# Optimization experiments

Measured on AMD Instinct MI355X. Metric: run time of the kernel, lower is better.

The kernel has to match this reference:

```python
import jax, jax.numpy as jnp
import numpy as np

N_NODES = 100000
N_EDGES = 3200000
IN_DIM = 128
HID = 16
MEM = 16
N_LAYERS = 2
OUT = 2
SLOPE = 0.01  # torch leaky_relu default negative_slope


def setup_inputs() -> dict:
    key = jax.random.key(0)
    ks = jax.random.split(key, 20)
    s = 0.05
    inp = {
        "x": jax.random.normal(ks[0], (N_NODES, IN_DIM), dtype=jnp.float32),
        "edge_index": jax.random.randint(ks[1], (2, N_EDGES), 0, N_NODES, dtype=jnp.int64),
        # preprocess MLP: Linear(input_dim,256) -> Linear(256,hidden)
        "pre1_W": jax.random.normal(ks[2], (256, IN_DIM), dtype=jnp.float32) * s,
        "pre1_b": jax.random.normal(ks[3], (256,), dtype=jnp.float32) * s,
        "pre2_W": jax.random.normal(ks[4], (HID, 256), dtype=jnp.float32) * s,
        "pre2_b": jax.random.normal(ks[5], (HID,), dtype=jnp.float32) * s,
        # per-layer hypernetwork GRU biases (input & initial hidden are zeros, so
        # only biases affect the GRU step) and weight_transform Linear(mem, hid*hid)
        "gru_bih": jax.random.normal(ks[6], (N_LAYERS, 3 * MEM), dtype=jnp.float32) * s,
        "gru_bhh": jax.random.normal(ks[7], (N_LAYERS, 3 * MEM), dtype=jnp.float32) * s,
        "wt_W": jax.random.normal(ks[8], (N_LAYERS, HID * HID, MEM), dtype=jnp.float32) * s,
        "wt_b": jax.random.normal(ks[9], (N_LAYERS, HID * HID), dtype=jnp.float32) * s,
        # GCNConv bias (kept as its own parameter in PyG; lin has bias=False)
        "gcn_b": jax.random.normal(ks[10], (N_LAYERS, HID), dtype=jnp.float32) * s,
        # postprocess heads
        "post1_W": jax.random.normal(ks[11], (OUT, HID), dtype=jnp.float32) * s,
        "post1_b": jax.random.normal(ks[12], (OUT,), dtype=jnp.float32) * s,
        "posta_W": jax.random.normal(ks[13], (1, HID), dtype=jnp.float32) * s,
        "posta_b": jax.random.normal(ks[14], (1,), dtype=jnp.float32) * s,
    }
    return inp


def _hyper_gcn_weight(bih, bhh, wt_W, wt_b):
    # GRU single step with zero input and zero initial hidden state:
    # only the biases contribute.  h' = (1-z)*n + z*h_prev, h_prev = 0.
    r = jax.nn.sigmoid(bih[:MEM] + bhh[:MEM])
    z = jax.nn.sigmoid(bih[MEM:2 * MEM] + bhh[MEM:2 * MEM])
    n = jnp.tanh(bih[2 * MEM:] + r * bhh[2 * MEM:])
    mem = (1.0 - z) * n  # [MEM]
    # weight_transform Linear -> view as lin.weight [out, in]; detached in torch
    W = (wt_W @ mem + wt_b).reshape(HID, HID)
    return jax.lax.stop_gradient(W)


def reference(x, edge_index, pre1_W, pre1_b, pre2_W, pre2_b, gru_bih, gru_bhh,
              wt_W, wt_b, gcn_b, post1_W, post1_b, posta_W, posta_b):
    N = x.shape[0]
    # preprocess (dropout p=0.0 -> identity)
    h = jax.nn.leaky_relu(x @ pre1_W.T + pre1_b, negative_slope=SLOPE)
    h = jax.nn.leaky_relu(h @ pre2_W.T + pre2_b, negative_slope=SLOPE)

    # GCN normalization with self-loops (PyG gcn_norm)
    src, dst = edge_index[0], edge_index[1]
    loops = jnp.arange(N, dtype=src.dtype)
    s = jnp.concatenate([src, loops])
    d = jnp.concatenate([dst, loops])
    deg = jax.ops.segment_sum(jnp.ones_like(d, dtype=h.dtype), d, num_segments=N)
    dinv = jnp.where(deg > 0, jax.lax.rsqrt(deg), 0.0)
    norm = dinv[s] * dinv[d]  # [E+N]

    for l in range(N_LAYERS):
        W = _hyper_gcn_weight(gru_bih[l], gru_bhh[l], wt_W[l], wt_b[l])
        xw = h @ W.T                                   # [N, HID]
        msg = xw[s] * norm[:, None]                    # gather + scale
        h = jax.ops.segment_sum(msg, d, num_segments=N) + gcn_b[l]
        h = jax.nn.leaky_relu(h, negative_slope=SLOPE)

    out = jnp.sum(h @ post1_W.T + post1_b, axis=-1)          # [N]
    anomaly = (h @ posta_W.T + posta_b)[:, 0]                # [N]
    return out, anomaly, h
```

## Files before the change

kernel.cpp:

```cpp
#include <hip/hip_runtime.h>
#include <hip/hip_bf16.h>
#include <math.h>

#define IN_DIM 128
#define PRE_HID 256
#define HID 16

__device__ __forceinline__ float lrelu(float v) { return v > 0.f ? v : 0.01f * v; }
__device__ __forceinline__ float fin(float v) { return (v == v && fabsf(v) < 1e30f) ? v : 0.f; }

__device__ __forceinline__ float ldp(const void* p, size_t i, int f32) {
    if (f32) return ((const float*)p)[i];
    unsigned u = ((const unsigned short*)p)[i];
    return __uint_as_float(u << 16);
}
__device__ __forceinline__ unsigned short f2bf(float f) {
    union { __hip_bfloat16 b; unsigned short u; } cv;
    cv.b = __float2bfloat16(f);
    return cv.u;
}
__device__ __forceinline__ void unpack8(uint4 u, float* o) {
    o[0] = __uint_as_float(u.x << 16); o[1] = __uint_as_float(u.x & 0xFFFF0000u);
    o[2] = __uint_as_float(u.y << 16); o[3] = __uint_as_float(u.y & 0xFFFF0000u);
    o[4] = __uint_as_float(u.z << 16); o[5] = __uint_as_float(u.z & 0xFFFF0000u);
    o[6] = __uint_as_float(u.w << 16); o[7] = __uint_as_float(u.w & 0xFFFF0000u);
}
__device__ __forceinline__ unsigned pk2(float a, float b) {
    return (unsigned)f2bf(a) | ((unsigned)f2bf(b) << 16);
}
__device__ __forceinline__ uint4 pack8(const float* v) {
    uint4 u;
    u.x = pk2(v[0], v[1]); u.y = pk2(v[2], v[3]);
    u.z = pk2(v[4], v[5]); u.w = pk2(v[6], v[7]);
    return u;
}

#define OFF_W1F   0
#define OFF_B1F   32768
#define OFF_W2T   33024
#define OFF_B2F   37120
#define OFF_HW    37136
#define OFF_GCNB  37648
#define OFF_POST  37680
#define OFF_FLAGS 37720
#define OFF_BSUM  37760
#define OFF_BPRE  37888
#define OFF_A0    38016

__global__ void k_detect(const unsigned short* __restrict__ xu,
                         const int* __restrict__ ei32, int* __restrict__ flags) {
    if (threadIdx.x == 0 && blockIdx.x == 0) {
        int band = 0;
        for (int k = 0; k < 128; ++k) {
            unsigned e = (xu[2 * k] >> 7) & 0xFF;
            if (e >= 100 && e <= 140) band++;
        }
        flags[1] = (band < 96) ? 1 : 0;
        int any = 0;
        for (int k = 0; k < 64; ++k) any |= ei32[2 * k + 1];
        flags[0] = (any == 0) ? 1 : 0;
    }
}

__global__ void k_sentinel(unsigned* __restrict__ out, int words, unsigned val) {
    int i = blockIdx.x * 256 + threadIdx.x;
    if (i < words) out[i] = val;
}

__global__ void k_prep_small(const void* __restrict__ bih, const void* __restrict__ bhh,
                             const void* __restrict__ wtW, const void* __restrict__ wtb,
                             const void* __restrict__ p1W, const void* __restrict__ p1b,
                             const void* __restrict__ paW, const void* __restrict__ pab,
                             const int* __restrict__ flags,
                             float* __restrict__ hw, float* __restrict__ post) {
    int f32 = flags[1];
    __shared__ float mem[2][16];
    int t = threadIdx.x;
    if (t < 32) {
        int l = t >> 4, j = t & 15;
        float bi0 = ldp(bih, l * 48 + j, f32),      bh0 = ldp(bhh, l * 48 + j, f32);
        float bi1 = ldp(bih, l * 48 + 16 + j, f32), bh1 = ldp(bhh, l * 48 + 16 + j, f32);
        float bi2 = ldp(bih, l * 48 + 32 + j, f32), bh2 = ldp(bhh, l * 48 + 32 + j, f32);
        float r = 1.f / (1.f + expf(-(bi0 + bh0)));
        float z = 1.f / (1.f + expf(-(bi1 + bh1)));
        float nn = tanhf(bi2 + r * bh2);
        mem[l][j] = (1.f - z) * nn;
    }
    __syncthreads();
    for (int l = 0; l < 2; ++l) {
        float acc = ldp(wtb, l * 256 + t, f32);
        #pragma unroll
        for (int m = 0; m < 16; ++m)
            acc += ldp(wtW, l * 4096 + t * 16 + m, f32) * mem[l][m];
        hw[l * 256 + t] = acc;
    }
    if (t < 16) {
        post[t]      = ldp(p1W, t, f32) + ldp(p1W, 16 + t, f32);
        post[17 + t] = ldp(paW, t, f32);
    }
    if (t == 0) {
        post[16] = ldp(p1b, 0, f32) + ldp(p1b, 1, f32);
        post[33] = ldp(pab, 0, f32);
    }
}

__global__ void k_convert(const void* __restrict__ p1W, const void* __restrict__ p1b,
                          const void* __restrict__ p2W, const void* __restrict__ p2b,
                          const void* __restrict__ gcnb, const int* __restrict__ flags,
                          float* __restrict__ w1f, float* __restrict__ b1f,
                          float* __restrict__ w2t, float* __restrict__ b2f,
                          float* __restrict__ gcnbf) {
    int f32 = flags[1];
    int i = blockIdx.x * 256 + threadIdx.x;
    if (i < 32768) w1f[i] = ldp(p1W, i, f32);
    if (i < 256)   b1f[i] = ldp(p1b, i, f32);
    if (i < 4096)  { int r = i >> 4, j = i & 15; w2t[i] = ldp(p2W, j * 256 + r, f32); }
    if (i < 16)    b2f[i] = ldp(p2b, i, f32);
    if (i < 32)    gcnbf[i] = ldp(gcnb, i, f32);
}

__global__ void k_deg(const int* __restrict__ ei, const int* __restrict__ flags,
                      unsigned* __restrict__ deg, int E, int N) {
    int e = blockIdx.x * 256 + threadIdx.x;
    if (e >= E) return;
    int d = flags[0] ? ei[2 * ((size_t)E + e)] : ei[(size_t)E + e];
    if ((unsigned)d < (unsigned)N) atomicAdd(&deg[d], 1u);
}

__global__ void k_dinv(float* __restrict__ degdinv, int N) {
    int n = blockIdx.x * 256 + threadIdx.x;
    if (n >= N) return;
    unsigned dg = ((unsigned*)degdinv)[n];
    degdinv[n] = 1.f / sqrtf((float)dg + 1.f);
}

__global__ void k_dinv2(const unsigned* __restrict__ deg, float* __restrict__ dinv, int N) {
    int n = blockIdx.x * 256 + threadIdx.x;
    if (n >= N) return;
    dinv[n] = 1.f / sqrtf((float)deg[n] + 1.f);
}

__global__ __launch_bounds__(1024) void k_scan_block(const unsigned* __restrict__ deg,
                                                     unsigned* __restrict__ bsum, int N) {
    __shared__ unsigned s[1024];
    int t = threadIdx.x;
    int i = blockIdx.x * 1024 + t;
    s[t] = (i < N) ? deg[i] : 0u;
    __syncthreads();
    for (int off = 512; off > 0; off >>= 1) {
        if (t < off) s[t] += s[t + off];
        __syncthreads();
    }
    if (t == 0) bsum[blockIdx.x] = s[0];
}

__global__ __launch_bounds__(128) void k_scan_top(unsigned* __restrict__ bsum,
                                                  unsigned* __restrict__ bpre, int NB) {
    __shared__ unsigned s[128];
    int t = threadIdx.x;
    unsigned v = (t < NB) ? bsum[t] : 0u;
    s[t] = v;
    __syncthreads();
    for (int off = 1; off < 128; off <<= 1) {
        unsigned a = (t >= off) ? s[t - off] : 0u;
        __syncthreads();
        s[t] += a;
        __syncthreads();
    }
    if (t < NB) bpre[t] = s[t] - v;
}

__global__ __launch_bounds__(1024) void k_scan_final(const unsigned* __restrict__ deg,
                                                     const unsigned* __restrict__ bpre,
                                                     unsigned* __restrict__ rowptr, int N) {
    __shared__ unsigned s[1024];
    int t = threadIdx.x;
    int i = blockIdx.x * 1024 + t;
    unsigned v = (i < N) ? deg[i] : 0u;
    s[t] = v;
    __syncthreads();
    for (int off = 1; off < 1024; off <<= 1) {
        unsigned a = (t >= off) ? s[t - off] : 0u;
        __syncthreads();
        s[t] += a;
        __syncthreads();
    }
    if (i < N) rowptr[i] = bpre[blockIdx.x] + s[t] - v;
}

__global__ void k_fill(const int* __restrict__ ei, const int* __restrict__ flags,
                       unsigned* __restrict__ rowptr, unsigned* __restrict__ csr,
                       int E, int N) {
    int e = blockIdx.x * 256 + threadIdx.x;
    if (e >= E) return;
    int s, d;
    if (flags[0]) { s = ei[2 * (size_t)e]; d = ei[2 * ((size_t)E + e)]; }
    else          { s = ei[e];             d = ei[(size_t)E + e]; }
    if ((unsigned)d >= (unsigned)N) return;
    if ((unsigned)s >= (unsigned)N) s = d;
    unsigned pos = atomicAdd(&rowptr[d], 1u);
    csr[pos] = (unsigned)s;
}

__global__ __launch_bounds__(256) void k_pre(const void* __restrict__ x,
                                             const float* __restrict__ w1f,
                                             const float* __restrict__ b1f,
                                             const float* __restrict__ w2t,
                                             const float* __restrict__ b2f,
                                             const int* __restrict__ flags,
                                             float* __restrict__ h, int N) {
    __shared__ unsigned short xs[64 * 128];
    __shared__ float pacc[192 * 16];
    const int t = threadIdx.x;
    const int base = blockIdx.x * 64;
    const int f32 = flags[1];
    #pragma unroll
    for (int i = 0; i < 4; ++i) {
        int id = i * 256 + t;
        int row = id >> 4, c = id & 15;
        uint4 v = make_uint4(0u, 0u, 0u, 0u);
        if (base + row < N) {
            if (f32) {
                const float* xp = (const float*)x + ((size_t)(base + row) << 7) + c * 8;
                float4 a = *reinterpret_cast<const float4*>(xp);
                float4 b = *reinterpret_cast<const float4*>(xp + 4);
                v.x = pk2(a.x, a.y); v.y = pk2(a.z, a.w);
                v.z = pk2(b.x, b.y); v.w = pk2(b.z, b.w);
            } else {
                v = *reinterpret_cast<const uint4*>((const unsigned short*)x +
                                                    ((size_t)(base + row) << 7) + c * 8);
            }
        }
        int cs = c ^ (row & 15);
        *reinterpret_cast<uint4*>(xs + row * 128 + cs * 8) = v;
    }
    __syncthreads();

    const int node = t & 63;
    const int half = t >> 6;
    const int rowbase = half * 64;
    const int nm = node & 15;

    float acc2[HID];
    #pragma unroll
    for (int j = 0; j < HID; ++j) acc2[j] = (half == 0) ? b2f[j] : 0.f;

    for (int rt = 0; rt < 8; ++rt) {
        const int r0 = rowbase + rt * 8;
        float s[8];
        #pragma unroll
        for (int r = 0; r < 8; ++r) s[r] = b1f[r0 + r];
        #pragma unroll 4
        for (int kc = 0; kc < 16; ++kc) {
            int cs = kc ^ nm;
            uint4 u = *reinterpret_cast<const uint4*>(xs + node * 128 + cs * 8);
            float xr[8];
            unpack8(u, xr);
            const float* wbase = w1f + (size_t)r0 * IN_DIM + kc * 8;
            #pragma unroll
            for (int r = 0; r < 8; ++r) {
                const float* wr = wbase + (size_t)r * IN_DIM;
                float acc = s[r];
                #pragma unroll
                for (int k = 0; k < 8; ++k) acc += wr[k] * xr[k];
                s[r] = acc;
            }
        }
        const float* w2base = w2t + (size_t)r0 * HID;
        #pragma unroll
        for (int r = 0; r < 8; ++r) {
            float v = lrelu(s[r]);
            const float* w2r = w2base + (size_t)r * HID;
            #pragma unroll
            for (int j = 0; j < HID; ++j) acc2[j] += w2r[j] * v;
        }
    }

    if (half != 0) {
        float* pp = pacc + ((half - 1) * 64 + node) * 16;
        #pragma unroll
        for (int j = 0; j < HID; ++j) pp[j] = acc2[j];
    }
    __syncthreads();
    if (half == 0 && base + node < N) {
        const float* p0 = pacc + node * 16;
        const float* p1 = pacc + (64 + node) * 16;
        const float* p2 = pacc + (128 + node) * 16;
        float4* hp = reinterpret_cast<float4*>(h + (size_t)(base + node) * HID);
        #pragma unroll
        for (int q = 0; q < 4; ++q) {
            float4 v;
            v.x = lrelu(acc2[q*4+0] + p0[q*4+0] + p1[q*4+0] + p2[q*4+0]);
            v.y = lrelu(acc2[q*4+1] + p0[q*4+1] + p1[q*4+1] + p2[q*4+1]);
            v.z = lrelu(acc2[q*4+2] + p0[q*4+2] + p1[q*4+2] + p2[q*4+2]);
            v.w = lrelu(acc2[q*4+3] + p0[q*4+3] + p1[q*4+3] + p2[q*4+3]);
            hp[q] = v;
        }
    }
}

__global__ void k_xw_y(const float* __restrict__ h, const float* __restrict__ W,
                       const float* __restrict__ dinv, float* __restrict__ y, int N) {
    int n = blockIdx.x * 256 + threadIdx.x;
    if (n >= N) return;
    float hv[HID];
    const float4* hp = reinterpret_cast<const float4*>(h + (size_t)n * HID);
    #pragma unroll
    for (int q = 0; q < 4; ++q) {
        float4 v = hp[q];
        hv[q*4+0] = v.x; hv[q*4+1] = v.y; hv[q*4+2] = v.z; hv[q*4+3] = v.w;
    }
    float dn = dinv[n];
    float4* yp = reinterpret_cast<float4*>(y + (size_t)n * HID);
    #pragma unroll
    for (int q = 0; q < 4; ++q) {
        float o[4];
        #pragma unroll
        for (int ii = 0; ii < 4; ++ii) {
            int i = q * 4 + ii;
            float s = 0.f;
            #pragma unroll
            for (int j = 0; j < HID; ++j) s += W[i * HID + j] * hv[j];
            o[ii] = s * dn;
        }
        float4 v; v.x = o[0]; v.y = o[1]; v.z = o[2]; v.w = o[3];
        yp[q] = v;
    }
}

__global__ __launch_bounds__(256) void k_gather(const unsigned* __restrict__ rowptr,
                                                const unsigned* __restrict__ deg,
                                                const unsigned* __restrict__ csr,
                                                const float* __restrict__ y,
                                                const float* __restrict__ dinv,
                                                const float* __restrict__ gcnbf,
                                                float* __restrict__ h, int N) {
    int tid = blockIdx.x * 256 + threadIdx.x;
    if (tid >= N * 4) return;
    int n = tid >> 2, q = tid & 3;
    unsigned end = rowptr[n];
    unsigned start = end - deg[n];
    float4 acc = *reinterpret_cast<const float4*>(y + (size_t)n * HID + q * 4);
    unsigned k = start;
    if (k < end) {
        unsigned src = csr[k];
        for (++k; k < end; ++k) {
            unsigned nxt = csr[k];
            float4 v = *reinterpret_cast<const float4*>(y + (size_t)src * HID + q * 4);
            acc.x += v.x; acc.y += v.y; acc.z += v.z; acc.w += v.w;
            src = nxt;
        }
        float4 v = *reinterpret_cast<const float4*>(y + (size_t)src * HID + q * 4);
        acc.x += v.x; acc.y += v.y; acc.z += v.z; acc.w += v.w;
    }
    float dn = dinv[n];
    float4 o;
    o.x = lrelu(fin(dn * acc.x) + gcnbf[q*4+0]);
    o.y = lrelu(fin(dn * acc.y) + gcnbf[q*4+1]);
    o.z = lrelu(fin(dn * acc.z) + gcnbf[q*4+2]);
    o.w = lrelu(fin(dn * acc.w) + gcnbf[q*4+3]);
    *reinterpret_cast<float4*>(h + (size_t)n * HID + q * 4) = o;
}

__global__ __launch_bounds__(256) void k_gather_final(const unsigned* __restrict__ rowptr,
                                                      const unsigned* __restrict__ deg,
                                                      const unsigned* __restrict__ csr,
                                                      const float* __restrict__ y,
                                                      const float* __restrict__ dinv,
                                                      const float* __restrict__ gcnbf,
                                                      const float* __restrict__ post,
                                                      const int* __restrict__ flags,
                                                      void* __restrict__ out, int N) {
    int tid = blockIdx.x * 256 + threadIdx.x;
    if (tid >= N * 4) return;
    int n = tid >> 2, q = tid & 3;
    unsigned end = rowptr[n];
    unsigned start = end - deg[n];
    float4 acc = *reinterpret_cast<const float4*>(y + (size_t)n * HID + q * 4);
    unsigned k = start;
    if (k < end) {
        unsigned src = csr[k];
        for (++k; k < end; ++k) {
            unsigned nxt = csr[k];
            float4 v = *reinterpret_cast<const float4*>(y + (size_t)src * HID + q * 4);
            acc.x += v.x; acc.y += v.y; acc.z += v.z; acc.w += v.w;
            src = nxt;
        }
        float4 v = *reinterpret_cast<const float4*>(y + (size_t)src * HID + q * 4);
        acc.x += v.x; acc.y += v.y; acc.z += v.z; acc.w += v.w;
    }
    float dn = dinv[n];
    float v0 = lrelu(fin(dn * acc.x) + gcnbf[q*4+0]);
    float v1 = lrelu(fin(dn * acc.y) + gcnbf[q*4+1]);
    float v2 = lrelu(fin(dn * acc.z) + gcnbf[q*4+2]);
    float v3 = lrelu(fin(dn * acc.w) + gcnbf[q*4+3]);
    float s1 = v0 * post[q*4+0] + v1 * post[q*4+1] + v2 * post[q*4+2] + v3 * post[q*4+3];
    float s2 = v0 * post[17+q*4+0] + v1 * post[17+q*4+1] + v2 * post[17+q*4+2] + v3 * post[17+q*4+3];
    #pragma unroll
    for (int m = 1; m < 4; m <<= 1) {
        s1 += __shfl_xor(s1, m, 64);
        s2 += __shfl_xor(s2, m, 64);
    }
    if (flags[1]) {
        float* ob = (float*)out;
        if (q == 0) ob[n] = s1 + post[16];
        if (q == 1) ob[N + n] = s2 + post[33];
        float4 o; o.x = v0; o.y = v1; o.z = v2; o.w = v3;
        *reinterpret_cast<float4*>(ob + 2 * (size_t)N + (size_t)n * HID + q * 4) = o;
    } else {
        unsigned short* ob = (unsigned short*)out;
        if (q == 0) ob[n] = f2bf(s1 + post[16]);
        if (q == 1) ob[N + n] = f2bf(s2 + post[33]);
        uint2 u; u.x = pk2(v0, v1); u.y = pk2(v2, v3);
        *reinterpret_cast<uint2*>(ob + 2 * (size_t)N + (size_t)n * HID + q * 4) = u;
    }
}

__global__ void k_xw(const float* __restrict__ h, const float* __restrict__ W,
                     const float* __restrict__ dinv, const int* __restrict__ flags,
                     void* __restrict__ xw, float* __restrict__ hacc, int N) {
    int n = blockIdx.x * 256 + threadIdx.x;
    if (n >= N) return;
    float hv[HID];
    const float4* hp = reinterpret_cast<const float4*>(h + (size_t)n * HID);
    #pragma unroll
    for (int q = 0; q < 4; ++q) {
        float4 v = hp[q];
        hv[q*4+0] = v.x; hv[q*4+1] = v.y; hv[q*4+2] = v.z; hv[q*4+3] = v.w;
    }
    float dn = dinv[n];
    float sl = dn * dn;
    float o[HID];
    #pragma unroll
    for (int i = 0; i < HID; ++i) {
        float s = 0.f;
        #pragma unroll
        for (int j = 0; j < HID; ++j) s += W[i * HID + j] * hv[j];
        o[i] = s;
    }
    if (flags[1]) {
        float4* xp = reinterpret_cast<float4*>((float*)xw + (size_t)n * HID);
        #pragma unroll
        for (int q = 0; q < 4; ++q) {
            float4 v; v.x = o[q*4+0]; v.y = o[q*4+1]; v.z = o[q*4+2]; v.w = o[q*4+3];
            xp[q] = v;
        }
    } else {
        uint4* xp = reinterpret_cast<uint4*>((unsigned short*)xw + (size_t)n * HID);
        xp[0] = pack8(o);
        xp[1] = pack8(o + 8);
    }
    float4* ap = reinterpret_cast<float4*>(hacc + (size_t)n * HID);
    #pragma unroll
    for (int q = 0; q < 4; ++q) {
        float4 va;
        va.x = o[q*4+0]*sl; va.y = o[q*4+1]*sl; va.z = o[q*4+2]*sl; va.w = o[q*4+3]*sl;
        ap[q] = va;
    }
}

__global__ __launch_bounds__(256) void k_scatter(const int* __restrict__ ei,
                                                 const int* __restrict__ flags,
                                                 const float* __restrict__ dinv,
                                                 const void* __restrict__ xw,
                                                 float* __restrict__ hacc, int E, int N) {
    int e = blockIdx.x * 256 + threadIdx.x;
    if (e >= E) return;
    int s, d;
    if (flags[0]) { s = ei[2 * (size_t)e]; d = ei[2 * ((size_t)E + e)]; }
    else          { s = ei[e];             d = ei[(size_t)E + e]; }
    if ((unsigned)s >= (unsigned)N || (unsigned)d >= (unsigned)N) return;
    float nrm = dinv[s] * dinv[d];
    float v[HID];
    if (flags[1]) {
        const float4* xr = reinterpret_cast<const float4*>((const float*)xw + (size_t)s * HID);
        #pragma unroll
        for (int q = 0; q < 4; ++q) {
            float4 a = xr[q];
            v[q*4+0] = a.x; v[q*4+1] = a.y; v[q*4+2] = a.z; v[q*4+3] = a.w;
        }
    } else {
        const uint4* xr = reinterpret_cast<const uint4*>((const unsigned short*)xw + (size_t)s * HID);
        unpack8(xr[0], v);
        unpack8(xr[1], v + 8);
    }
    float* out = hacc + (size_t)d * HID;
    #pragma unroll
    for (int j = 0; j < HID; ++j) unsafeAtomicAdd(out + j, v[j] * nrm);
}

__global__ void k_finish(const float* __restrict__ hacc, const float* __restrict__ gcnbf,
                         float* __restrict__ h, int N) {
    int n = blockIdx.x * 256 + threadIdx.x;
    if (n >= N) return;
    const float4* ap = reinterpret_cast<const float4*>(hacc + (size_t)n * HID);
    float4* hp = reinterpret_cast<float4*>(h + (size_t)n * HID);
    #pragma unroll
    for (int q = 0; q < 4; ++q) {
        float4 a = ap[q];
        float4 o;
        o.x = lrelu(fin(a.x) + gcnbf[q*4+0]);
        o.y = lrelu(fin(a.y) + gcnbf[q*4+1]);
        o.z = lrelu(fin(a.z) + gcnbf[q*4+2]);
        o.w = lrelu(fin(a.w) + gcnbf[q*4+3]);
        hp[q] = o;
    }
}

__global__ void k_final(const float* __restrict__ hacc, const float* __restrict__ gcnbf,
                        const float* __restrict__ post, const int* __restrict__ flags,
                        void* __restrict__ out, int N) {
    int n = blockIdx.x * 256 + threadIdx.x;
    if (n >= N) return;
    float v[HID];
    const float4* ap = reinterpret_cast<const float4*>(hacc + (size_t)n * HID);
    #pragma unroll
    for (int q = 0; q < 4; ++q) {
        float4 a = ap[q];
        v[q*4+0] = lrelu(fin(a.x) + gcnbf[q*4+0]);
        v[q*4+1] = lrelu(fin(a.y) + gcnbf[q*4+1]);
        v[q*4+2] = lrelu(fin(a.z) + gcnbf[q*4+2]);
        v[q*4+3] = lrelu(fin(a.w) + gcnbf[q*4+3]);
    }
    float o = post[16], an = post[33];
    #pragma unroll
    for (int j = 0; j < HID; ++j) {
        o += v[j] * post[j];
        an += v[j] * post[17 + j];
    }
    if (flags[1]) {
        float* ob = (float*)out;
        ob[n] = o;
        ob[N + n] = an;
        float* hr = ob + 2 * (size_t)N + (size_t)n * HID;
        #pragma unroll
        for (int j = 0; j < HID; ++j) hr[j] = v[j];
    } else {
        unsigned short* ob = (unsigned short*)out;
        ob[n] = f2bf(o);
        ob[N + n] = f2bf(an);
        uint4* hr = reinterpret_cast<uint4*>(ob + 2 * (size_t)N + (size_t)n * HID);
        hr[0] = pack8(v);
        hr[1] = pack8(v + 8);
    }
}

extern "C" void kernel_launch(void* const* d_in, const int* in_sizes, int n_in,
                              void* d_out, int out_size, void* d_ws, size_t ws_size,
                              hipStream_t stream) {
    const void* x    = d_in[0];
    const int*  ei   = (const int*)d_in[1];
    const void* p1W  = d_in[2];
    const void* p1b  = d_in[3];
    const void* p2W  = d_in[4];
    const void* p2b  = d_in[5];
    const void* bih  = d_in[6];
    const void* bhh  = d_in[7];
    const void* wtW  = d_in[8];
    const void* wtb  = d_in[9];
    const void* gcnb = d_in[10];
    const void* po1W = d_in[11];
    const void* po1b = d_in[12];
    const void* poaW = d_in[13];
    const void* poab = d_in[14];

    const int N = in_sizes[0] / IN_DIM;
    const int E = in_sizes[1] / 2;

    float* ws = (float*)d_ws;
    float* w1f   = ws + OFF_W1F;
    float* b1f   = ws + OFF_B1F;
    float* w2t   = ws + OFF_W2T;
    float* b2f   = ws + OFF_B2F;
    float* hw    = ws + OFF_HW;
    float* gcnbf = ws + OFF_GCNB;
    float* post  = ws + OFF_POST;
    int*   flags = (int*)(ws + OFF_FLAGS);
    unsigned* bsum = (unsigned*)(ws + OFF_BSUM);
    unsigned* bpre = (unsigned*)(ws + OFF_BPRE);

    const int nb_nodes = (N + 255) / 256;
    const int nb_edges = (E + 255) / 256;
    const int nb_n4    = (N * 4 + 255) / 256;
    const int nb_pre   = (N + 63) / 64;
    const int NB       = (N + 1023) / 1024;

    size_t req_csr = ((size_t)OFF_A0 + 35 * (size_t)N + (size_t)E + 64) * 4;
    size_t req_fb  = ((size_t)OFF_A0 + 33 * (size_t)N + 64) * 4;

    if (ws_size >= req_csr && NB <= 128) {
        unsigned* deg    = (unsigned*)(ws + OFF_A0);
        unsigned* rowptr = deg + N;
        float*    dinv   = (float*)(rowptr + N);
        unsigned* csr    = (unsigned*)(dinv + N);
        float*    y      = (float*)(csr + E);
        float*    h      = y + (size_t)N * HID;

        hipMemsetAsync(deg, 0, (size_t)N * 4, stream);
        k_detect<<<1, 64, 0, stream>>>((const unsigned short*)x, ei, flags);
        k_prep_small<<<1, 256, 0, stream>>>(bih, bhh, wtW, wtb, po1W, po1b, poaW, poab,
                                            flags, hw, post);
        k_convert<<<128, 256, 0, stream>>>(p1W, p1b, p2W, p2b, gcnb, flags,
                                           w1f, b1f, w2t, b2f, gcnbf);
        k_deg<<<nb_edges, 256, 0, stream>>>(ei, flags, deg, E, N);
        k_dinv2<<<nb_nodes, 256, 0, stream>>>(deg, dinv, N);
        k_scan_block<<<NB, 1024, 0, stream>>>(deg, bsum, N);
        k_scan_top<<<1, 128, 0, stream>>>(bsum, bpre, NB);
        k_scan_final<<<NB, 1024, 0, stream>>>(deg, bpre, rowptr, N);
        k_fill<<<nb_edges, 256, 0, stream>>>(ei, flags, rowptr, csr, E, N);
        k_pre<<<nb_pre, 256, 0, stream>>>(x, w1f, b1f, w2t, b2f, flags, h, N);

        k_xw_y<<<nb_nodes, 256, 0, stream>>>(h, hw + 0, dinv, y, N);
        k_gather<<<nb_n4, 256, 0, stream>>>(rowptr, deg, csr, y, dinv, gcnbf + 0, h, N);
        k_xw_y<<<nb_nodes, 256, 0, stream>>>(h, hw + 256, dinv, y, N);
        k_gather_final<<<nb_n4, 256, 0, stream>>>(rowptr, deg, csr, y, dinv, gcnbf + 16,
                                                  post, flags, d_out, N);
    } else if (ws_size >= req_fb) {
        float* degdinv = ws + OFF_A0;
        float* hacc    = degdinv + N;
        float* h       = hacc + (size_t)N * HID;
        void*  xw      = d_out;

        hipMemsetAsync(degdinv, 0, (size_t)N * 4, stream);
        k_detect<<<1, 64, 0, stream>>>((const unsigned short*)x, ei, flags);
        k_prep_small<<<1, 256, 0, stream>>>(bih, bhh, wtW, wtb, po1W, po1b, poaW, poab,
                                            flags, hw, post);
        k_convert<<<128, 256, 0, stream>>>(p1W, p1b, p2W, p2b, gcnb, flags,
                                           w1f, b1f, w2t, b2f, gcnbf);
        k_deg<<<nb_edges, 256, 0, stream>>>(ei, flags, (unsigned*)degdinv, E, N);
        k_dinv<<<nb_nodes, 256, 0, stream>>>(degdinv, N);
        k_pre<<<nb_pre, 256, 0, stream>>>(x, w1f, b1f, w2t, b2f, flags, h, N);
        for (int l = 0; l < 2; ++l) {
            k_xw<<<nb_nodes, 256, 0, stream>>>(h, hw + l * 256, degdinv, flags, xw, hacc, N);
            k_scatter<<<nb_edges, 256, 0, stream>>>(ei, flags, degdinv, xw, hacc, E, N);
            if (l == 0) k_finish<<<nb_nodes, 256, 0, stream>>>(hacc, gcnbf + 0, h, N);
            else        k_final<<<nb_nodes, 256, 0, stream>>>(hacc, gcnbf + 16, post, flags, d_out, N);
        }
    } else {
        float f = 256.0f + (float)(ws_size >> 20);
        unsigned uv; __builtin_memcpy(&uv, &f, 4);
        int words = out_size / 2;
        k_sentinel<<<(words + 255) / 256, 256, 0, stream>>>((unsigned*)d_out, words, uv);
    }
}
```

Before: 1.130 ms.

## Fuse per-layer XW transform into preprocess and gather kernels

Folds the first layer's h·W and dinv scaling into the preprocess MLP kernel and the second layer's into the layer-1 gather epilogue, removing both k_xw_y launches and the h round trips through memory. The preprocess kernel also remaps threads so the four partial sums for a node sit in adjacent lanes and are combined with wavefront shuffles instead of shared memory and a barrier. The gather uses shuffles within groups of four lanes to assemble the full 16-wide row before the matvec. The costs are more register pressure and a change in the memory access pattern for x in shared memory (adjacent lanes now read different swizzled rows).

```diff
diff --git a/kernel.cpp b/kernel.cpp
--- a/kernel.cpp
+++ b/kernel.cpp
@@ -207,10 +207,11 @@
                                              const float* __restrict__ b1f,
                                              const float* __restrict__ w2t,
                                              const float* __restrict__ b2f,
+                                             const float* __restrict__ W0,
+                                             const float* __restrict__ dinv,
                                              const int* __restrict__ flags,
-                                             float* __restrict__ h, int N) {
+                                             float* __restrict__ y, int N) {
     __shared__ unsigned short xs[64 * 128];
-    __shared__ float pacc[192 * 16];
     const int t = threadIdx.x;
     const int base = blockIdx.x * 64;
     const int f32 = flags[1];
@@ -236,14 +237,14 @@
     }
     __syncthreads();
 
-    const int node = t & 63;
-    const int half = t >> 6;
+    const int node = t >> 2;
+    const int half = t & 3;
     const int rowbase = half * 64;
     const int nm = node & 15;
 
     float acc2[HID];
     #pragma unroll
-    for (int j = 0; j < HID; ++j) acc2[j] = (half == 0) ? b2f[j] : 0.f;
+    for (int j = 0; j < HID; ++j) acc2[j] = 0.f;
 
     for (int rt = 0; rt < 8; ++rt) {
         const int r0 = rowbase + rt * 8;
@@ -275,91 +276,87 @@
             for (int j = 0; j < HID; ++j) acc2[j] += w2r[j] * v;
         }
     }
-
-    if (half != 0) {
-        float* pp = pacc + ((half - 1) * 64 + node) * 16;
-        #pragma unroll
-        for (int j = 0; j < HID; ++j) pp[j] = acc2[j];
-    }
-    __syncthreads();
+    #pragma unroll
+    for (int j = 0; j < HID; ++j) {
+        acc2[j] += __shfl_xor(acc2[j], 1, 64);
+        acc2[j] += __shfl_xor(acc2[j], 2, 64);
+    }
     if (half == 0 && base + node < N) {
-        const float* p0 = pacc + node * 16;
-        const float* p1 = pacc + (64 + node) * 16;
-        const float* p2 = pacc + (128 + node) * 16;
-        float4* hp = reinterpret_cast<float4*>(h + (size_t)(base + node) * HID);
+        int n = base + node;
+        float hv[HID];
+        #pragma unroll
+        for (int j = 0; j < HID; ++j) hv[j] = lrelu(acc2[j] + b2f[j]);
+        float dn = dinv[n];
+        float4* yp = reinterpret_cast<float4*>(y + (size_t)n * HID);
         #pragma unroll
         for (int q = 0; q < 4; ++q) {
-            float4 v;
-            v.x = lrelu(acc2[q*4+0] + p0[q*4+0] + p1[q*4+0] + p2[q*4+0]);
-            v.y = lrelu(acc2[q*4+1] + p0[q*4+1] + p1[q*4+1] + p2[q*4+1]);
-            v.z = lrelu(acc2[q*4+2] + p0[q*4+2] + p1[q*4+2] + p2[q*4+2]);
-            v.w = lrelu(acc2[q*4+3] + p0[q*4+3] + p1[q*4+3] + p2[q*4+3]);
-            hp[q] = v;
-        }
-    }
-}
-
-__global__ void k_xw_y(const float* __restrict__ h, const float* __restrict__ W,
-                       const float* __restrict__ dinv, float* __restrict__ y, int N) {
-    int n = blockIdx.x * 256 + threadIdx.x;
-    if (n >= N) return;
-    float hv[HID];
-    const float4* hp = reinterpret_cast<const float4*>(h + (size_t)n * HID);
-    #pragma unroll
-    for (int q = 0; q < 4; ++q) {
-        float4 v = hp[q];
-        hv[q*4+0] = v.x; hv[q*4+1] = v.y; hv[q*4+2] = v.z; hv[q*4+3] = v.w;
-    }
-    float dn = dinv[n];
-    float4* yp = reinterpret_cast<float4*>(y + (size_t)n * HID);
-    #pragma unroll
-    for (int q = 0; q < 4; ++q) {
-        float o[4];
-        #pragma unroll
-        for (int ii = 0; ii < 4; ++ii) {
-            int i = q * 4 + ii;
-            float s = 0.f;
+            float o[4];
             #pragma unroll
-            for (int j = 0; j < HID; ++j) s += W[i * HID + j] * hv[j];
-            o[ii] = s * dn;
-        }
-        float4 v; v.x = o[0]; v.y = o[1]; v.z = o[2]; v.w = o[3];
-        yp[q] = v;
+            for (int ii = 0; ii < 4; ++ii) {
+                int i = q * 4 + ii;
+                float s = 0.f;
+                #pragma unroll
+                for (int j = 0; j < HID; ++j) s += W0[i * HID + j] * hv[j];
+                o[ii] = s * dn;
+            }
+            float4 v; v.x = o[0]; v.y = o[1]; v.z = o[2]; v.w = o[3];
+            yp[q] = v;
+        }
     }
 }
 
 __global__ __launch_bounds__(256) void k_gather(const unsigned* __restrict__ rowptr,
                                                 const unsigned* __restrict__ deg,
                                                 const unsigned* __restrict__ csr,
-                                                const float* __restrict__ y,
+                                                const float* __restrict__ ya,
                                                 const float* __restrict__ dinv,
                                                 const float* __restrict__ gcnbf,
-                                                float* __restrict__ h, int N) {
+                                                const float* __restrict__ W,
+                                                float* __restrict__ yb, int N) {
     int tid = blockIdx.x * 256 + threadIdx.x;
     if (tid >= N * 4) return;
     int n = tid >> 2, q = tid & 3;
     unsigned end = rowptr[n];
     unsigned start = end - deg[n];
-    float4 acc = *reinterpret_cast<const float4*>(y + (size_t)n * HID + q * 4);
+    float4 acc = *reinterpret_cast<const float4*>(ya + (size_t)n * HID + q * 4);
     unsigned k = start;
     if (k < end) {
         unsigned src = csr[k];
         for (++k; k < end; ++k) {
             unsigned nxt = csr[k];
-            float4 v = *reinterpret_cast<const float4*>(y + (size_t)src * HID + q * 4);
+            float4 v = *reinterpret_cast<const float4*>(ya + (size_t)src * HID + q * 4);
             acc.x += v.x; acc.y += v.y; acc.z += v.z; acc.w += v.w;
             src = nxt;
         }
-        float4 v = *reinterpret_cast<const float4*>(y + (size_t)src * HID + q * 4);
+        float4 v = *reinterpret_cast<const float4*>(ya + (size_t)src * HID + q * 4);
         acc.x += v.x; acc.y += v.y; acc.z += v.z; acc.w += v.w;
     }
     float dn = dinv[n];
-    float4 o;
-    o.x = lrelu(fin(dn * acc.x) + gcnbf[q*4+0]);
-    o.y = lrelu(fin(dn * acc.y) + gcnbf[q*4+1]);
-    o.z = lrelu(fin(dn * acc.z) + gcnbf[q*4+2]);
-    o.w = lrelu(fin(dn * acc.w) + gcnbf[q*4+3]);
-    *reinterpret_cast<float4*>(h + (size_t)n * HID + q * 4) = o;
+    float v0 = lrelu(fin(dn * acc.x) + gcnbf[q*4+0]);
+    float v1 = lrelu(fin(dn * acc.y) + gcnbf[q*4+1]);
+    float v2 = lrelu(fin(dn * acc.z) + gcnbf[q*4+2]);
+    float v3 = lrelu(fin(dn * acc.w) + gcnbf[q*4+3]);
+    int lb = (threadIdx.x & 63) & ~3;
+    float hrow[HID];
+    #pragma unroll
+    for (int k2 = 0; k2 < 4; ++k2) {
+        int sl = lb + k2;
+        hrow[k2*4+0] = __shfl(v0, sl, 64);
+        hrow[k2*4+1] = __shfl(v1, sl, 64);
+        hrow[k2*4+2] = __shfl(v2, sl, 64);
+        hrow[k2*4+3] = __shfl(v3, sl, 64);
+    }
+    float o[4];
+    #pragma unroll
+    for (int ii = 0; ii < 4; ++ii) {
+        int i = q * 4 + ii;
+        float s = 0.f;
+        #pragma unroll
+        for (int j = 0; j < HID; ++j) s += W[i * HID + j] * hrow[j];
+        o[ii] = s * dn;
+    }
+    float4 ov; ov.x = o[0]; ov.y = o[1]; ov.z = o[2]; ov.w = o[3];
+    *reinterpret_cast<float4*>(yb + (size_t)n * HID + q * 4) = ov;
 }
 
 __global__ __launch_bounds__(256) void k_gather_final(const unsigned* __restrict__ rowptr,
@@ -416,6 +413,99 @@
     }
 }
 
+__global__ __launch_bounds__(256) void k_pre_fb(const void* __restrict__ x,
+                                                const float* __restrict__ w1f,
+                                                const float* __restrict__ b1f,
+                                                const float* __restrict__ w2t,
+                                                const float* __restrict__ b2f,
+                                                const int* __restrict__ flags,
+                                                float* __restrict__ h, int N) {
+    __shared__ unsigned short xs[64 * 128];
+    __shared__ float pacc[192 * 16];
+    const int t = threadIdx.x;
+    const int base = blockIdx.x * 64;
+    const int f32 = flags[1];
+    #pragma unroll
+    for (int i = 0; i < 4; ++i) {
+        int id = i * 256 + t;
+        int row = id >> 4, c = id & 15;
+        uint4 v = make_uint4(0u, 0u, 0u, 0u);
+        if (base + row < N) {
+            if (f32) {
+                const float* xp = (const float*)x + ((size_t)(base + row) << 7) + c * 8;
+                float4 a = *reinterpret_cast<const float4*>(xp);
+                float4 b = *reinterpret_cast<const float4*>(xp + 4);
+                v.x = pk2(a.x, a.y); v.y = pk2(a.z, a.w);
+                v.z = pk2(b.x, b.y); v.w = pk2(b.z, b.w);
+            } else {
+                v = *reinterpret_cast<const uint4*>((const unsigned short*)x +
+                                                    ((size_t)(base + row) << 7) + c * 8);
+            }
+        }
+        int cs = c ^ (row & 15);
+        *reinterpret_cast<uint4*>(xs + row * 128 + cs * 8) = v;
+    }
+    __syncthreads();
+    const int node = t & 63;
+    const int half = t >> 6;
+    const int rowbase = half * 64;
+    const int nm = node & 15;
+    float acc2[HID];
+    #pragma unroll
+    for (int j = 0; j < HID; ++j) acc2[j] = (half == 0) ? b2f[j] : 0.f;
+    for (int rt = 0; rt < 8; ++rt) {
+        const int r0 = rowbase + rt * 8;
+        float s[8];
+        #pragma unroll
+        for (int r = 0; r < 8; ++r) s[r] = b1f[r0 + r];
+        #pragma unroll 4
+        for (int kc = 0; kc < 16; ++kc) {
+            int cs = kc ^ nm;
+            uint4 u = *reinterpret_cast<const uint4*>(xs + node * 128 + cs * 8);
+            float xr[8];
+            unpack8(u, xr);
+            const float* wbase = w1f + (size_t)r0 * IN_DIM + kc * 8;
+            #pragma unroll
+            for (int r = 0; r < 8; ++r) {
+                const float* wr = wbase + (size_t)r * IN_DIM;
+                float acc = s[r];
+                #pragma unroll
+                for (int k = 0; k < 8; ++k) acc += wr[k] * xr[k];
+                s[r] = acc;
+            }
+        }
+        const float* w2base = w2t + (size_t)r0 * HID;
+        #pragma unroll
+        for (int r = 0; r < 8; ++r) {
+            float v = lrelu(s[r]);
+            const float* w2r = w2base + (size_t)r * HID;
+            #pragma unroll
+            for (int j = 0; j < HID; ++j) acc2[j] += w2r[j] * v;
+        }
+    }
+    if (half != 0) {
+        float* pp = pacc + ((half - 1) * 64 + node) * 16;
+        #pragma unroll
+        for (int j = 0; j < HID; ++j) pp[j] = acc2[j];
+    }
+    __syncthreads();
+    if (half == 0 && base + node < N) {
+        const float* p0 = pacc + node * 16;
+        const float* p1 = pacc + (64 + node) * 16;
+        const float* p2 = pacc + (128 + node) * 16;
+        float4* hp = reinterpret_cast<float4*>(h + (size_t)(base + node) * HID);
+        #pragma unroll
+        for (int q = 0; q < 4; ++q) {
+            float4 v;
+            v.x = lrelu(acc2[q*4+0] + p0[q*4+0] + p1[q*4+0] + p2[q*4+0]);
+            v.y = lrelu(acc2[q*4+1] + p0[q*4+1] + p1[q*4+1] + p2[q*4+1]);
+            v.z = lrelu(acc2[q*4+2] + p0[q*4+2] + p1[q*4+2] + p2[q*4+2]);
+            v.w = lrelu(acc2[q*4+3] + p0[q*4+3] + p1[q*4+3] + p2[q*4+3]);
+            hp[q] = v;
+        }
+    }
+}
+
 __global__ void k_xw(const float* __restrict__ h, const float* __restrict__ W,
                      const float* __restrict__ dinv, const int* __restrict__ flags,
                      void* __restrict__ xw, float* __restrict__ hacc, int N) {
@@ -593,8 +683,8 @@
         unsigned* rowptr = deg + N;
         float*    dinv   = (float*)(rowptr + N);
         unsigned* csr    = (unsigned*)(dinv + N);
-        float*    y      = (float*)(csr + E);
-        float*    h      = y + (size_t)N * HID;
+        float*    ya     = (float*)(csr + E);
+        float*    yb     = ya + (size_t)N * HID;
 
         hipMemsetAsync(deg, 0, (size_t)N * 4, stream);
         k_detect<<<1, 64, 0, stream>>>((const unsigned short*)x, ei, flags);
@@ -608,12 +698,11 @@
         k_scan_top<<<1, 128, 0, stream>>>(bsum, bpre, NB);
         k_scan_final<<<NB, 1024, 0, stream>>>(deg, bpre, rowptr, N);
         k_fill<<<nb_edges, 256, 0, stream>>>(ei, flags, rowptr, csr, E, N);
-        k_pre<<<nb_pre, 256, 0, stream>>>(x, w1f, b1f, w2t, b2f, flags, h, N);
-
-        k_xw_y<<<nb_nodes, 256, 0, stream>>>(h, hw + 0, dinv, y, N);
-        k_gather<<<nb_n4, 256, 0, stream>>>(rowptr, deg, csr, y, dinv, gcnbf + 0, h, N);
-        k_xw_y<<<nb_nodes, 256, 0, stream>>>(h, hw + 256, dinv, y, N);
-        k_gather_final<<<nb_n4, 256, 0, stream>>>(rowptr, deg, csr, y, dinv, gcnbf + 16,
+        k_pre<<<nb_pre, 256, 0, stream>>>(x, w1f, b1f, w2t, b2f, hw + 0, dinv,
+                                          flags, ya, N);
+        k_gather<<<nb_n4, 256, 0, stream>>>(rowptr, deg, csr, ya, dinv, gcnbf + 0,
+                                            hw + 256, yb, N);
+        k_gather_final<<<nb_n4, 256, 0, stream>>>(rowptr, deg, csr, yb, dinv, gcnbf + 16,
                                                   post, flags, d_out, N);
     } else if (ws_size >= req_fb) {
         float* degdinv = ws + OFF_A0;
@@ -629,7 +718,7 @@
                                            w1f, b1f, w2t, b2f, gcnbf);
         k_deg<<<nb_edges, 256, 0, stream>>>(ei, flags, (unsigned*)degdinv, E, N);
         k_dinv<<<nb_nodes, 256, 0, stream>>>(degdinv, N);
-        k_pre<<<nb_pre, 256, 0, stream>>>(x, w1f, b1f, w2t, b2f, flags, h, N);
+        k_pre_fb<<<nb_pre, 256, 0, stream>>>(x, w1f, b1f, w2t, b2f, flags, h, N);
         for (int l = 0; l < 2; ++l) {
             k_xw<<<nb_nodes, 256, 0, stream>>>(h, hw + l * 256, degdinv, flags, xw, hacc, N);
             k_scatter<<<nb_edges, 256, 0, stream>>>(ei, flags, degdinv, xw, hacc, E, N);
```

Measured after the change: 2.426 ms. +114.7%, slower.
